# Optimization experiments

Measured on AMD Instinct MI355X. Metric: run time of the kernel, lower is better.

## Reference

```python
import jax, jax.numpy as jnp
import numpy as np
import math

D_MODEL = 1024
N_HEADS = 16
D_K = D_MODEL // N_HEADS


def setup_inputs() -> dict:
    key = jax.random.key(0)
    ks = jax.random.split(key, 9)
    B, N = 2, 8192
    s = 1.0 / math.sqrt(D_MODEL)
    x = jax.random.normal(ks[0], (B, N, D_MODEL), dtype=jnp.float32)
    Wq = jax.random.normal(ks[1], (D_MODEL, D_MODEL), dtype=jnp.float32) * s
    bq = jnp.zeros((D_MODEL,), dtype=jnp.float32)
    Wk = jax.random.normal(ks[2], (D_MODEL, D_MODEL), dtype=jnp.float32) * s
    bk = jnp.zeros((D_MODEL,), dtype=jnp.float32)
    Wv = jax.random.normal(ks[3], (D_MODEL, D_MODEL), dtype=jnp.float32) * s
    bv = jnp.zeros((D_MODEL,), dtype=jnp.float32)
    Wo = jax.random.normal(ks[4], (D_MODEL, D_MODEL), dtype=jnp.float32) * s
    bo = jnp.zeros((D_MODEL,), dtype=jnp.float32)
    return {"x": x, "Wq": Wq, "bq": bq, "Wk": Wk, "bk": bk,
            "Wv": Wv, "bv": bv, "Wo": Wo, "bo": bo}


def _fft_circulant_attention(Q, K, V):
    # Q,K,V: (B,H,N,d_k); FFT along the sequence axis (axis=2)
    B, H, N, d_k = Q.shape
    scale = 1.0 / math.sqrt(d_k)
    Q_fft = jnp.fft.rfft(Q, axis=2)
    K_fft = jnp.fft.rfft(K, axis=2)
    # circular cross-correlation summed over d_k -> (B,H,Nf)
    scores_fft = jnp.sum(Q_fft * jnp.conj(K_fft), axis=-1)
    scores = jnp.fft.irfft(scores_fft, n=N, axis=2) * scale  # (B,H,N)
    attn = jax.nn.softmax(scores, axis=-1)                    # (B,H,N)
    attn_fft = jnp.fft.rfft(attn, axis=2)                     # (B,H,Nf)
    V_fft = jnp.fft.rfft(V, axis=2)                           # (B,H,Nf,d_k)
    out_fft = attn_fft[..., None] * V_fft
    return jnp.fft.irfft(out_fft, n=N, axis=2)                # (B,H,N,d_k)


def reference(x, Wq, bq, Wk, bk, Wv, bv, Wo, bo):
    B, N, _ = x.shape
    # torch Linear: x @ W.T + b
    def proj(W, b):
        return (x @ W.T + b).reshape(B, N, N_HEADS, D_K).transpose(0, 2, 1, 3)
    Q = proj(Wq, bq)
    K = proj(Wk, bk)
    V = proj(Wv, bv)
    O = _fft_circulant_attention(Q, K, V)          # (B,H,N,d_k)
    O = O.transpose(0, 2, 1, 3).reshape(B, N, D_MODEL)
    return O @ Wo.T + bo
```

## Files before the change

kernel.cpp:

```cpp
#include <hip/hip_runtime.h>
#include <math.h>
#include <stdint.h>

#define NDIM 8192
#define LOG2N 13
#define DM 1024
#define NH 16
#define DKH 64
#define BATCH 2
#define NSPLIT 16
#define NPT (NDIM / 256)

typedef __attribute__((ext_vector_type(8))) short short8v;
typedef __attribute__((ext_vector_type(4))) float f32x4;

__device__ inline float bf2f(unsigned short u) {
  return __uint_as_float(((unsigned int)u) << 16);
}
__device__ inline unsigned short f2bf(float f) {
  unsigned int u = __float_as_uint(f);
  u += 0x7fffu + ((u >> 16) & 1u);
  return (unsigned short)(u >> 16);
}
__device__ inline float2 cmul(float2 a, float2 b) {
  return make_float2(a.x * b.x - a.y * b.y, a.x * b.y + a.y * b.x);
}
__device__ inline float2 cmulc(float2 a, float2 b) {
  return make_float2(a.x * b.x + a.y * b.y, a.y * b.x - a.x * b.y);
}

__device__ inline void gload_lds16(const void* g, void* l) {
  __builtin_amdgcn_global_load_lds(
      (const __attribute__((address_space(1))) unsigned int*)(uintptr_t)g,
      (__attribute__((address_space(3))) unsigned int*)(uintptr_t)l, 16, 0, 0);
}

__global__ void twiddle_init(float2* tw) {
  int k = blockIdx.x * blockDim.x + threadIdx.x;
  if (k < NDIM) {
    double a = -2.0 * 3.14159265358979323846 * (double)k / (double)NDIM;
    tw[k] = make_float2((float)cos(a), (float)sin(a));
  }
}

__global__ __launch_bounds__(256)
void split_x(const float* __restrict__ x, unsigned short* __restrict__ xhi,
             unsigned short* __restrict__ xlo) {
  size_t i = ((size_t)blockIdx.x * 256 + threadIdx.x) * 4;
  float4 v = *(const float4*)&x[i];
  ushort4 h, l;
  h.x = f2bf(v.x); l.x = f2bf(v.x - bf2f(h.x));
  h.y = f2bf(v.y); l.y = f2bf(v.y - bf2f(h.y));
  h.z = f2bf(v.z); l.z = f2bf(v.z - bf2f(h.z));
  h.w = f2bf(v.w); l.w = f2bf(v.w - bf2f(h.w));
  *(ushort4*)&xhi[i] = h;
  *(ushort4*)&xlo[i] = l;
}

__global__ __launch_bounds__(256)
void split_w(const float* __restrict__ Wq, const float* __restrict__ Wk,
             const float* __restrict__ Wv, const float* __restrict__ Wo,
             unsigned short* __restrict__ whi, unsigned short* __restrict__ wlo,
             unsigned short* __restrict__ wob) {
  int z = blockIdx.z;
  const float* W = (z == 0) ? Wq : ((z == 1) ? Wk : ((z == 2) ? Wv : Wo));
  size_t i = ((size_t)blockIdx.x * 256 + threadIdx.x) * 4;
  float4 v = *(const float4*)&W[i];
  ushort4 h, l;
  h.x = f2bf(v.x); l.x = f2bf(v.x - bf2f(h.x));
  h.y = f2bf(v.y); l.y = f2bf(v.y - bf2f(h.y));
  h.z = f2bf(v.z); l.z = f2bf(v.z - bf2f(h.z));
  h.w = f2bf(v.w); l.w = f2bf(v.w - bf2f(h.w));
  if (z < 3) {
    *(ushort4*)&whi[(size_t)z * DM * DM + i] = h;
    *(ushort4*)&wlo[(size_t)z * DM * DM + i] = l;
  } else {
    *(ushort4*)&wob[i] = h;
  }
}

__device__ inline void fft_fwd(float2* __restrict__ s, const float2* __restrict__ tw, int tid) {
  for (int lm = 11; lm >= 1; lm -= 2) {
    int m = 1 << lm;
    int sh = 11 - lm;
    __syncthreads();
    for (int t = tid; t < NDIM / 4; t += 256) {
      int p = t & (m - 1);
      int i0 = ((t >> lm) << (lm + 2)) + p;
      float2 x0 = s[i0], x1 = s[i0 + m], x2 = s[i0 + 2 * m], x3 = s[i0 + 3 * m];
      float2 a = make_float2(x0.x + x2.x, x0.y + x2.y);
      float2 b = make_float2(x0.x - x2.x, x0.y - x2.y);
      float2 c = make_float2(x1.x + x3.x, x1.y + x3.y);
      float2 d = make_float2(x1.x - x3.x, x1.y - x3.y);
      float2 y0 = make_float2(a.x + c.x, a.y + c.y);
      float2 y2 = make_float2(a.x - c.x, a.y - c.y);
      float2 y1 = make_float2(b.x + d.y, b.y - d.x);
      float2 y3 = make_float2(b.x - d.y, b.y + d.x);
      int e = p << sh;
      s[i0] = y0;
      s[i0 + m]     = cmul(y1, tw[e]);
      s[i0 + 2 * m] = cmul(y2, tw[2 * e]);
      s[i0 + 3 * m] = cmul(y3, tw[3 * e]);
    }
  }
  __syncthreads();
  for (int t = tid; t < NDIM / 2; t += 256) {
    int i0 = t * 2;
    float2 u = s[i0], v = s[i0 + 1];
    s[i0] = make_float2(u.x + v.x, u.y + v.y);
    s[i0 + 1] = make_float2(u.x - v.x, u.y - v.y);
  }
  __syncthreads();
}
__device__ inline void fft_inv(float2* __restrict__ s, const float2* __restrict__ tw, int tid) {
  __syncthreads();
  for (int t = tid; t < NDIM / 2; t += 256) {
    int i0 = t * 2;
    float2 u = s[i0], v = s[i0 + 1];
    s[i0] = make_float2(u.x + v.x, u.y + v.y);
    s[i0 + 1] = make_float2(u.x - v.x, u.y - v.y);
  }
  for (int lm = 1; lm <= 11; lm += 2) {
    int m = 1 << lm;
    int sh = 11 - lm;
    __syncthreads();
    for (int t = tid; t < NDIM / 4; t += 256) {
      int p = t & (m - 1);
      int i0 = ((t >> lm) << (lm + 2)) + p;
      int e = p << sh;
      float2 z0 = s[i0];
      float2 z1 = cmulc(s[i0 + m], tw[e]);
      float2 z2 = cmulc(s[i0 + 2 * m], tw[2 * e]);
      float2 z3 = cmulc(s[i0 + 3 * m], tw[3 * e]);
      float2 a = make_float2(z0.x + z2.x, z0.y + z2.y);
      float2 b = make_float2(z0.x - z2.x, z0.y - z2.y);
      float2 c = make_float2(z1.x + z3.x, z1.y + z3.y);
      float2 d = make_float2(z1.x - z3.x, z1.y - z3.y);
      s[i0]         = make_float2(a.x + c.x, a.y + c.y);
      s[i0 + m]     = make_float2(b.x - d.y, b.y + d.x);
      s[i0 + 2 * m] = make_float2(a.x - c.x, a.y - c.y);
      s[i0 + 3 * m] = make_float2(b.x + d.y, b.y - d.x);
    }
  }
  __syncthreads();
}

__device__ inline float blk_max(float v, float* red, int tid) {
  #pragma unroll
  for (int o = 32; o > 0; o >>= 1) v = fmaxf(v, __shfl_down(v, o, 64));
  __syncthreads();
  if ((tid & 63) == 0) red[tid >> 6] = v;
  __syncthreads();
  float r = fmaxf(fmaxf(red[0], red[1]), fmaxf(red[2], red[3]));
  __syncthreads();
  return r;
}
__device__ inline float blk_sum(float v, float* red, int tid) {
  #pragma unroll
  for (int o = 32; o > 0; o >>= 1) v += __shfl_down(v, o, 64);
  __syncthreads();
  if ((tid & 63) == 0) red[tid >> 6] = v;
  __syncthreads();
  float r = (red[0] + red[1]) + (red[2] + red[3]);
  __syncthreads();
  return r;
}

__global__ __launch_bounds__(256)
void proj_gemm_mfma(const unsigned short* __restrict__ xhi, const unsigned short* __restrict__ xlo,
                    const unsigned short* __restrict__ whi, const unsigned short* __restrict__ wlo,
                    const float* __restrict__ bq, const float* __restrict__ bk,
                    const float* __restrict__ bv,
                    float* __restrict__ Qt, float* __restrict__ Kt, unsigned short* __restrict__ Vt) {
  int z = blockIdx.z;
  int b = z / 3, wsel = z % 3;
  bool full = (wsel < 2);
  const unsigned short* Wh = whi + (size_t)wsel * DM * DM;
  const unsigned short* Wl = wlo + (size_t)wsel * DM * DM;
  const float* bias = (wsel == 0) ? bq : ((wsel == 1) ? bk : bv);
  int cb = blockIdx.y * 128;
  int nb = blockIdx.x * 128;
  __shared__ unsigned short lAh[128 * 64], lAl[128 * 64];
  __shared__ unsigned short lBh[128 * 64], lBl[128 * 64];
  int tid = threadIdx.x;
  int lane = tid & 63, wid = tid >> 6;
  int wr = wid >> 1, wc = wid & 1;
  int srow = tid >> 3, sg = tid & 7;
  const unsigned short* gAh = Wh + (size_t)cb * DM;
  const unsigned short* gAl = Wl + (size_t)cb * DM;
  const unsigned short* gBh = xhi + ((size_t)b * NDIM + nb) * DM;
  const unsigned short* gBl = xlo + ((size_t)b * NDIM + nb) * DM;

  f32x4 acc[4][4];
  #pragma unroll
  for (int i = 0; i < 4; ++i)
    #pragma unroll
    for (int j = 0; j < 4; ++j) acc[i][j] = (f32x4){0.f, 0.f, 0.f, 0.f};

  int col = lane & 15, kg = lane >> 4;
  for (int k0 = 0; k0 < DM; k0 += 64) {
    #pragma unroll
    for (int i = 0; i < 4; ++i) {
      int r = i * 32 + srow;
      int gc = (sg ^ (r & 7)) * 8;
      size_t go = (size_t)r * DM + k0 + gc;
      int lo_ = r * 64 + sg * 8;
      gload_lds16(gAh + go, &lAh[lo_]);
      gload_lds16(gBh + go, &lBh[lo_]);
      if (full) {
        gload_lds16(gAl + go, &lAl[lo_]);
        gload_lds16(gBl + go, &lBl[lo_]);
      }
    }
    asm volatile("s_waitcnt vmcnt(0)");
    __syncthreads();
    #pragma unroll
    for (int kk = 0; kk < 2; ++kk) {
      short8v ah[4], al[4], bh_[4], bl_[4];
      #pragma unroll
      for (int mi = 0; mi < 4; ++mi) {
        int r = wr * 64 + mi * 16 + col;
        int s = r * 64 + (((kk * 4 + kg) ^ (r & 7)) * 8);
        ah[mi] = *(const short8v*)&lAh[s];
        if (full) al[mi] = *(const short8v*)&lAl[s];
      }
      #pragma unroll
      for (int ni = 0; ni < 4; ++ni) {
        int r = wc * 64 + ni * 16 + col;
        int s = r * 64 + (((kk * 4 + kg) ^ (r & 7)) * 8);
        bh_[ni] = *(const short8v*)&lBh[s];
        if (full) bl_[ni] = *(const short8v*)&lBl[s];
      }
      #pragma unroll
      for (int mi = 0; mi < 4; ++mi)
        #pragma unroll
        for (int ni = 0; ni < 4; ++ni) {
          acc[mi][ni] = __builtin_amdgcn_mfma_f32_16x16x32_bf16(ah[mi], bh_[ni], acc[mi][ni], 0, 0, 0);
          if (full) {
            acc[mi][ni] = __builtin_amdgcn_mfma_f32_16x16x32_bf16(ah[mi], bl_[ni], acc[mi][ni], 0, 0, 0);
            acc[mi][ni] = __builtin_amdgcn_mfma_f32_16x16x32_bf16(al[mi], bh_[ni], acc[mi][ni], 0, 0, 0);
          }
        }
    }
    __syncthreads();
  }
  size_t obase = (size_t)b * DM * NDIM;
  #pragma unroll
  for (int mi = 0; mi < 4; ++mi) {
    #pragma unroll
    for (int reg = 0; reg < 4; ++reg) {
      int c = cb + wr * 64 + mi * 16 + kg * 4 + reg;
      float bsv = bias[c];
      #pragma unroll
      for (int ni = 0; ni < 4; ++ni) {
        int n = nb + wc * 64 + ni * 16 + col;
        float v = acc[mi][ni][reg] + bsv;
        if (wsel < 2) {
          float* out = ((wsel == 0) ? Qt : Kt) + obase;
          out[(size_t)c * NDIM + n] = v;
        } else {
          Vt[obase + (size_t)c * NDIM + n] = f2bf(v);
        }
      }
    }
  }
}

__global__ __launch_bounds__(256)
void score_fft_kernel(const float* __restrict__ Qt, const float* __restrict__ Kt,
                      const float2* __restrict__ tw, float2* __restrict__ part) {
  extern __shared__ float2 buf[];
  int bh = blockIdx.x / NSPLIT;
  int split = blockIdx.x % NSPLIT;
  int b = bh / NH, h = bh % NH;
  int tid = threadIdx.x;
  float qfx[NPT], qfy[NPT], accx[NPT], accy[NPT];
  #pragma unroll
  for (int i = 0; i < NPT; ++i) { accx[i] = 0.f; accy[i] = 0.f; }

  for (int dp = 0; dp < 2; ++dp) {
    int c0 = h * DKH + (split * 2 + dp) * 2;
    const float* q0 = Qt + ((size_t)b * DM + c0) * NDIM;
    const float* q1 = q0 + NDIM;
    const float* k0c = Kt + ((size_t)b * DM + c0) * NDIM;
    const float* k1c = k0c + NDIM;
    #pragma unroll
    for (int i = 0; i < NPT; ++i) {
      int ii = i * 256 + tid;
      buf[ii] = make_float2(q0[ii], q1[ii]);
    }
    fft_fwd(buf, tw, tid);
    #pragma unroll
    for (int i = 0; i < NPT; ++i) { float2 v = buf[i * 256 + tid]; qfx[i] = v.x; qfy[i] = v.y; }
    #pragma unroll
    for (int i = 0; i < NPT; ++i) {
      int ii = i * 256 + tid;
      buf[ii] = make_float2(k0c[ii], k1c[ii]);
    }
    fft_fwd(buf, tw, tid);
    #pragma unroll
    for (int i = 0; i < NPT; ++i) {
      float2 kf = buf[i * 256 + tid];
      accx[i] += qfx[i] * kf.x + qfy[i] * kf.y;
      accy[i] += qfy[i] * kf.x - qfx[i] * kf.y;
    }
  }
  float2* dst = part + ((size_t)bh * NSPLIT + split) * NDIM;
  #pragma unroll
  for (int i = 0; i < NPT; ++i) dst[i * 256 + tid] = make_float2(accx[i], accy[i]);
}

__global__ __launch_bounds__(256)
void softmax_attn_kernel(const float2* __restrict__ part, const float2* __restrict__ tw,
                         float2* __restrict__ attnf) {
  extern __shared__ float2 buf[];
  int bh = blockIdx.x;
  int tid = threadIdx.x;
  for (int i = tid; i < NDIM; i += 256) {
    float sx = 0.f, sy = 0.f;
    #pragma unroll
    for (int s = 0; s < NSPLIT; ++s) {
      float2 v = part[((size_t)bh * NSPLIT + s) * NDIM + i];
      sx += v.x; sy += v.y;
    }
    buf[i] = make_float2(sx, sy);
  }
  fft_inv(buf, tw, tid);
  const float scale = 0.125f / (float)NDIM;
  float vals[NPT];
  float lmax = -3.0e38f;
  #pragma unroll
  for (int i = 0; i < NPT; ++i) {
    float v = buf[i * 256 + tid].x * scale;
    vals[i] = v;
    lmax = fmaxf(lmax, v);
  }
  float* red = (float*)buf;
  float gmax = blk_max(lmax, red, tid);
  float lsum = 0.f;
  #pragma unroll
  for (int i = 0; i < NPT; ++i) { float e = expf(vals[i] - gmax); vals[i] = e; lsum += e; }
  float gsum = blk_sum(lsum, red, tid);
  float inv = 1.0f / gsum;
  #pragma unroll
  for (int i = 0; i < NPT; ++i) buf[i * 256 + tid] = make_float2(vals[i] * inv, 0.f);
  fft_fwd(buf, tw, tid);
  for (int i = tid; i < NDIM; i += 256) attnf[(size_t)bh * NDIM + i] = buf[i];
}

__global__ __launch_bounds__(256)
void out_fft_kernel(const unsigned short* __restrict__ Vt, const float2* __restrict__ attnf,
                    const float2* __restrict__ tw, unsigned short* __restrict__ Ot) {
  extern __shared__ float2 buf[];
  int idx = blockIdx.x;
  int b = idx / (DM / 2), cp = idx % (DM / 2);
  int c0 = cp * 2;
  int h = c0 >> 6;
  int bh = b * NH + h;
  int tid = threadIdx.x;
  const unsigned short* v0 = Vt + ((size_t)b * DM + c0) * NDIM;
  const unsigned short* v1 = v0 + NDIM;
  for (int i = tid; i < NDIM; i += 256) buf[i] = make_float2(bf2f(v0[i]), bf2f(v1[i]));
  fft_fwd(buf, tw, tid);
  for (int i = tid; i < NDIM; i += 256) {
    float2 vf = buf[i];
    float2 af = attnf[(size_t)bh * NDIM + i];
    buf[i] = cmul(vf, af);
  }
  fft_inv(buf, tw, tid);
  const float invn = 1.0f / (float)NDIM;
  unsigned short* o0 = Ot + ((size_t)b * DM + c0) * NDIM;
  unsigned short* o1 = o0 + NDIM;
  for (int i = tid; i < NDIM; i += 256) {
    float2 v = buf[i];
    o0[i] = f2bf(v.x * invn);
    o1[i] = f2bf(v.y * invn);
  }
}

__global__ __launch_bounds__(256)
void transpose_ot(const unsigned short* __restrict__ Ot, unsigned short* __restrict__ Ont) {
  int b = blockIdx.z;
  int cb = blockIdx.y * 64, n0 = blockIdx.x * 64;
  __shared__ unsigned short t[64][68];
  int tid = threadIdx.x;
  int r = tid >> 4, c4 = (tid & 15) * 4;
  const unsigned short* src = Ot + (size_t)b * DM * NDIM;
  #pragma unroll
  for (int i = 0; i < 4; ++i) {
    ushort4 v = *(const ushort4*)&src[(size_t)(cb + i * 16 + r) * NDIM + n0 + c4];
    *(ushort4*)&t[i * 16 + r][c4] = v;
  }
  __syncthreads();
  unsigned short* dst = Ont + (size_t)b * NDIM * DM;
  #pragma unroll
  for (int i = 0; i < 4; ++i) {
    int n = i * 16 + r;
    ushort4 v;
    v.x = t[c4 + 0][n]; v.y = t[c4 + 1][n]; v.z = t[c4 + 2][n]; v.w = t[c4 + 3][n];
    *(ushort4*)&dst[(size_t)(n0 + n) * DM + cb + c4] = v;
  }
}

__global__ __launch_bounds__(256)
void final_gemm_mfma(const unsigned short* __restrict__ Ont, const unsigned short* __restrict__ Wob,
                     const float* __restrict__ bo, float* __restrict__ out) {
  int b = blockIdx.z;
  int nb = blockIdx.x * 128;
  int pb = blockIdx.y * 128;
  __shared__ unsigned short lA[128 * 64], lB[128 * 64];
  int tid = threadIdx.x;
  int lane = tid & 63, wid = tid >> 6;
  int wr = wid >> 1, wc = wid & 1;
  int srow = tid >> 3, sg = tid & 7;
  const unsigned short* gA = Ont + ((size_t)b * NDIM + nb) * DM;
  const unsigned short* gB = Wob + (size_t)pb * DM;

  f32x4 acc[4][4];
  #pragma unroll
  for (int i = 0; i < 4; ++i)
    #pragma unroll
    for (int j = 0; j < 4; ++j) acc[i][j] = (f32x4){0.f, 0.f, 0.f, 0.f};

  int col = lane & 15, kg = lane >> 4;
  for (int k0 = 0; k0 < DM; k0 += 64) {
    #pragma unroll
    for (int i = 0; i < 4; ++i) {
      int r = i * 32 + srow;
      int gc = (sg ^ (r & 7)) * 8;
      size_t go = (size_t)r * DM + k0 + gc;
      int lo_ = r * 64 + sg * 8;
      gload_lds16(gA + go, &lA[lo_]);
      gload_lds16(gB + go, &lB[lo_]);
    }
    asm volatile("s_waitcnt vmcnt(0)");
    __syncthreads();
    #pragma unroll
    for (int kk = 0; kk < 2; ++kk) {
      short8v af[4], bf[4];
      #pragma unroll
      for (int mi = 0; mi < 4; ++mi) {
        int r = wr * 64 + mi * 16 + col;
        af[mi] = *(const short8v*)&lA[r * 64 + (((kk * 4 + kg) ^ (r & 7)) * 8)];
      }
      #pragma unroll
      for (int ni = 0; ni < 4; ++ni) {
        int r = wc * 64 + ni * 16 + col;
        bf[ni] = *(const short8v*)&lB[r * 64 + (((kk * 4 + kg) ^ (r & 7)) * 8)];
      }
      #pragma unroll
      for (int mi = 0; mi < 4; ++mi)
        #pragma unroll
        for (int ni = 0; ni < 4; ++ni)
          acc[mi][ni] = __builtin_amdgcn_mfma_f32_16x16x32_bf16(af[mi], bf[ni], acc[mi][ni], 0, 0, 0);
    }
    __syncthreads();
  }
  #pragma unroll
  for (int mi = 0; mi < 4; ++mi) {
    #pragma unroll
    for (int reg = 0; reg < 4; ++reg) {
      int n = nb + wr * 64 + mi * 16 + kg * 4 + reg;
      size_t rowoff = ((size_t)b * NDIM + n) * DM;
      #pragma unroll
      for (int ni = 0; ni < 4; ++ni) {
        int cp = pb + wc * 64 + ni * 16 + col;
        out[rowoff + cp] = acc[mi][ni][reg] + bo[cp];
      }
    }
  }
}

extern "C" void kernel_launch(void* const* d_in, const int* in_sizes, int n_in,
                              void* d_out, int out_size, void* d_ws, size_t ws_size,
                              hipStream_t stream) {
  (void)in_sizes; (void)n_in; (void)out_size;
  const float* x  = (const float*)d_in[0];
  const float* Wq = (const float*)d_in[1]; const float* bq = (const float*)d_in[2];
  const float* Wk = (const float*)d_in[3]; const float* bk = (const float*)d_in[4];
  const float* Wv = (const float*)d_in[5]; const float* bv = (const float*)d_in[6];
  const float* Wo = (const float*)d_in[7]; const float* bo = (const float*)d_in[8];

  char* ws = (char*)d_ws;
  size_t off = 0;
  float2* tw = (float2*)(ws + off); off += (size_t)NDIM * sizeof(float2);
  float*  Qt = (float*)(ws + off);  off += (size_t)BATCH * DM * NDIM * 4;
  float*  Kt = (float*)(ws + off);  off += (size_t)BATCH * DM * NDIM * 4;
  unsigned short* Vt  = (unsigned short*)(ws + off); off += (size_t)BATCH * DM * NDIM * 2;
  size_t xhi_off = off;
  unsigned short* Xhi = (unsigned short*)(ws + off); off += (size_t)BATCH * NDIM * DM * 2;
  size_t xlo_off = off;
  unsigned short* Xlo = (unsigned short*)(ws + off); off += (size_t)BATCH * NDIM * DM * 2;
  unsigned short* Whi = (unsigned short*)(ws + off); off += (size_t)3 * DM * DM * 2;
  unsigned short* Wlo = (unsigned short*)(ws + off); off += (size_t)3 * DM * DM * 2;
  unsigned short* Wob = (unsigned short*)(ws + off); off += (size_t)DM * DM * 2;
  float2* part  = (float2*)(ws + xhi_off);
  float2* attnf = (float2*)(ws + xlo_off);
  unsigned short* Ot  = (unsigned short*)Qt;
  unsigned short* Ont = (unsigned short*)Kt;

  if (ws_size < off) return;

  twiddle_init<<<32, 256, 0, stream>>>(tw);
  split_x<<<(BATCH * NDIM * DM) / (256 * 4), 256, 0, stream>>>(x, Xhi, Xlo);
  split_w<<<dim3((DM * DM) / (256 * 4), 1, 4), 256, 0, stream>>>(Wq, Wk, Wv, Wo, Whi, Wlo, Wob);

  dim3 pg(NDIM / 128, DM / 128, 3 * BATCH);
  proj_gemm_mfma<<<pg, 256, 0, stream>>>(Xhi, Xlo, Whi, Wlo, bq, bk, bv, Qt, Kt, Vt);

  score_fft_kernel<<<BATCH * NH * NSPLIT, 256, NDIM * sizeof(float2), stream>>>(Qt, Kt, tw, part);
  softmax_attn_kernel<<<BATCH * NH, 256, NDIM * sizeof(float2), stream>>>(part, tw, attnf);
  out_fft_kernel<<<BATCH * DM / 2, 256, NDIM * sizeof(float2), stream>>>(Vt, attnf, tw, Ot);

  transpose_ot<<<dim3(NDIM / 64, DM / 64, BATCH), 256, 0, stream>>>(Ot, Ont);
  final_gemm_mfma<<<dim3(NDIM / 128, DM / 128, BATCH), 256, 0, stream>>>(Ont, Wob, bo, (float*)d_out);
}
```

Baseline: 528.9 us.

## Use radix-8 FFT stages and split partial-sum reduction into its own kernel

Replaces the radix-4 shared-memory FFT passes with radix-8 butterflies, so the 8192-point transform takes four radix-8 passes plus a radix-2 pass instead of six radix-4 passes plus a radix-2 pass. This means fewer barriers and fewer LDS round trips per FFT, at the cost of more registers per thread. Separately, the sum over split partial score spectra moves out of the 32-block softmax kernel into a wide grid-parallel reduction kernel. That spreads the memory-bound reduction across many more CUs, but adds an extra kernel launch and an intermediate buffer.

```diff
diff --git a/kernel.cpp b/kernel.cpp
--- a/kernel.cpp
+++ b/kernel.cpp
@@ -3,7 +3,6 @@
 #include <stdint.h>
 
 #define NDIM 8192
-#define LOG2N 13
 #define DM 1024
 #define NH 16
 #define DKH 64
@@ -80,66 +79,100 @@
 }
 
 __device__ inline void fft_fwd(float2* __restrict__ s, const float2* __restrict__ tw, int tid) {
-  for (int lm = 11; lm >= 1; lm -= 2) {
+  const float C = 0.70710678118654752f;
+  for (int lm = 10; lm >= 1; lm -= 3) {
     int m = 1 << lm;
-    int sh = 11 - lm;
+    int sh = 10 - lm;
     __syncthreads();
-    for (int t = tid; t < NDIM / 4; t += 256) {
+    for (int t = tid; t < NDIM / 8; t += 256) {
       int p = t & (m - 1);
-      int i0 = ((t >> lm) << (lm + 2)) + p;
-      float2 x0 = s[i0], x1 = s[i0 + m], x2 = s[i0 + 2 * m], x3 = s[i0 + 3 * m];
-      float2 a = make_float2(x0.x + x2.x, x0.y + x2.y);
-      float2 b = make_float2(x0.x - x2.x, x0.y - x2.y);
-      float2 c = make_float2(x1.x + x3.x, x1.y + x3.y);
-      float2 d = make_float2(x1.x - x3.x, x1.y - x3.y);
-      float2 y0 = make_float2(a.x + c.x, a.y + c.y);
-      float2 y2 = make_float2(a.x - c.x, a.y - c.y);
-      float2 y1 = make_float2(b.x + d.y, b.y - d.x);
-      float2 y3 = make_float2(b.x - d.y, b.y + d.x);
+      int i0 = ((t >> lm) << (lm + 3)) + p;
+      float2 x0 = s[i0],       x1 = s[i0 + m],     x2 = s[i0 + 2 * m], x3 = s[i0 + 3 * m];
+      float2 x4 = s[i0 + 4 * m], x5 = s[i0 + 5 * m], x6 = s[i0 + 6 * m], x7 = s[i0 + 7 * m];
+      float2 e0 = {x0.x + x4.x, x0.y + x4.y}, o0 = {x0.x - x4.x, x0.y - x4.y};
+      float2 e1 = {x1.x + x5.x, x1.y + x5.y}, o1 = {x1.x - x5.x, x1.y - x5.y};
+      float2 e2 = {x2.x + x6.x, x2.y + x6.y}, o2 = {x2.x - x6.x, x2.y - x6.y};
+      float2 e3 = {x3.x + x7.x, x3.y + x7.y}, o3 = {x3.x - x7.x, x3.y - x7.y};
+      float2 t1 = {C * (o1.x + o1.y), C * (o1.y - o1.x)};
+      float2 t2 = {o2.y, -o2.x};
+      float2 t3 = {C * (o3.y - o3.x), -C * (o3.x + o3.y)};
+      float2 pe = {e0.x + e2.x, e0.y + e2.y}, qe = {e0.x - e2.x, e0.y - e2.y};
+      float2 re = {e1.x + e3.x, e1.y + e3.y}, se = {e1.x - e3.x, e1.y - e3.y};
+      float2 po = {o0.x + t2.x, o0.y + t2.y}, qo = {o0.x - t2.x, o0.y - t2.y};
+      float2 ro = {t1.x + t3.x, t1.y + t3.y}, so = {t1.x - t3.x, t1.y - t3.y};
+      float2 y0 = {pe.x + re.x, pe.y + re.y};
+      float2 y4 = {pe.x - re.x, pe.y - re.y};
+      float2 y2 = {qe.x + se.y, qe.y - se.x};
+      float2 y6 = {qe.x - se.y, qe.y + se.x};
+      float2 y1 = {po.x + ro.x, po.y + ro.y};
+      float2 y5 = {po.x - ro.x, po.y - ro.y};
+      float2 y3 = {qo.x + so.y, qo.y - so.x};
+      float2 y7 = {qo.x - so.y, qo.y + so.x};
       int e = p << sh;
-      s[i0] = y0;
+      s[i0]         = y0;
       s[i0 + m]     = cmul(y1, tw[e]);
       s[i0 + 2 * m] = cmul(y2, tw[2 * e]);
       s[i0 + 3 * m] = cmul(y3, tw[3 * e]);
+      s[i0 + 4 * m] = cmul(y4, tw[4 * e]);
+      s[i0 + 5 * m] = cmul(y5, tw[5 * e]);
+      s[i0 + 6 * m] = cmul(y6, tw[6 * e]);
+      s[i0 + 7 * m] = cmul(y7, tw[7 * e]);
     }
   }
   __syncthreads();
   for (int t = tid; t < NDIM / 2; t += 256) {
     int i0 = t * 2;
     float2 u = s[i0], v = s[i0 + 1];
-    s[i0] = make_float2(u.x + v.x, u.y + v.y);
+    s[i0]     = make_float2(u.x + v.x, u.y + v.y);
     s[i0 + 1] = make_float2(u.x - v.x, u.y - v.y);
   }
   __syncthreads();
 }
+
 __device__ inline void fft_inv(float2* __restrict__ s, const float2* __restrict__ tw, int tid) {
+  const float C = 0.70710678118654752f;
   __syncthreads();
   for (int t = tid; t < NDIM / 2; t += 256) {
     int i0 = t * 2;
     float2 u = s[i0], v = s[i0 + 1];
-    s[i0] = make_float2(u.x + v.x, u.y + v.y);
+    s[i0]     = make_float2(u.x + v.x, u.y + v.y);
     s[i0 + 1] = make_float2(u.x - v.x, u.y - v.y);
   }
-  for (int lm = 1; lm <= 11; lm += 2) {
+  for (int lm = 1; lm <= 10; lm += 3) {
     int m = 1 << lm;
-    int sh = 11 - lm;
+    int sh = 10 - lm;
     __syncthreads();
-    for (int t = tid; t < NDIM / 4; t += 256) {
+    for (int t = tid; t < NDIM / 8; t += 256) {
       int p = t & (m - 1);
-      int i0 = ((t >> lm) << (lm + 2)) + p;
+      int i0 = ((t >> lm) << (lm + 3)) + p;
       int e = p << sh;
       float2 z0 = s[i0];
-      float2 z1 = cmulc(s[i0 + m], tw[e]);
+      float2 z1 = cmulc(s[i0 + m],     tw[e]);
       float2 z2 = cmulc(s[i0 + 2 * m], tw[2 * e]);
       float2 z3 = cmulc(s[i0 + 3 * m], tw[3 * e]);
-      float2 a = make_float2(z0.x + z2.x, z0.y + z2.y);
-      float2 b = make_float2(z0.x - z2.x, z0.y - z2.y);
-      float2 c = make_float2(z1.x + z3.x, z1.y + z3.y);
-      float2 d = make_float2(z1.x - z3.x, z1.y - z3.y);
-      s[i0]         = make_float2(a.x + c.x, a.y + c.y);
-      s[i0 + m]     = make_float2(b.x - d.y, b.y + d.x);
-      s[i0 + 2 * m] = make_float2(a.x - c.x, a.y - c.y);
-      s[i0 + 3 * m] = make_float2(b.x + d.y, b.y - d.x);
+      float2 z4 = cmulc(s[i0 + 4 * m], tw[4 * e]);
+      float2 z5 = cmulc(s[i0 + 5 * m], tw[5 * e]);
+      float2 z6 = cmulc(s[i0 + 6 * m], tw[6 * e]);
+      float2 z7 = cmulc(s[i0 + 7 * m], tw[7 * e]);
+      float2 E0 = {z0.x + z4.x, z0.y + z4.y}, O0 = {z0.x - z4.x, z0.y - z4.y};
+      float2 E1 = {z1.x + z5.x, z1.y + z5.y}, O1 = {z1.x - z5.x, z1.y - z5.y};
+      float2 E2 = {z2.x + z6.x, z2.y + z6.y}, O2 = {z2.x - z6.x, z2.y - z6.y};
+      float2 E3 = {z3.x + z7.x, z3.y + z7.y}, O3 = {z3.x - z7.x, z3.y - z7.y};
+      float2 T1 = {C * (O1.x - O1.y), C * (O1.x + O1.y)};
+      float2 T2 = {-O2.y, O2.x};
+      float2 T3 = {-C * (O3.x + O3.y), C * (O3.x - O3.y)};
+      float2 PE = {E0.x + E2.x, E0.y + E2.y}, QE = {E0.x - E2.x, E0.y - E2.y};
+      float2 RE = {E1.x + E3.x, E1.y + E3.y}, SE = {E1.x - E3.x, E1.y - E3.y};
+      float2 PO = {O0.x + T2.x, O0.y + T2.y}, QO = {O0.x - T2.x, O0.y - T2.y};
+      float2 RO = {T1.x + T3.x, T1.y + T3.y}, SO = {T1.x - T3.x, T1.y - T3.y};
+      s[i0]         = make_float2(PE.x + RE.x, PE.y + RE.y);
+      s[i0 + 4 * m] = make_float2(PE.x - RE.x, PE.y - RE.y);
+      s[i0 + 2 * m] = make_float2(QE.x - SE.y, QE.y + SE.x);
+      s[i0 + 6 * m] = make_float2(QE.x + SE.y, QE.y - SE.x);
+      s[i0 + m]     = make_float2(PO.x + RO.x, PO.y + RO.y);
+      s[i0 + 5 * m] = make_float2(PO.x - RO.x, PO.y - RO.y);
+      s[i0 + 3 * m] = make_float2(QO.x - SO.y, QO.y + SO.x);
+      s[i0 + 7 * m] = make_float2(QO.x + SO.y, QO.y - SO.x);
     }
   }
   __syncthreads();
@@ -311,20 +344,29 @@
 }
 
 __global__ __launch_bounds__(256)
-void softmax_attn_kernel(const float2* __restrict__ part, const float2* __restrict__ tw,
+void reduce_part(const float2* __restrict__ part, float2* __restrict__ sred) {
+  #pragma unroll
+  for (int rep = 0; rep < 2; ++rep) {
+    size_t g = (size_t)blockIdx.x * 512 + rep * 256 + threadIdx.x;
+    int bh = (int)(g >> 13);
+    int i  = (int)(g & (NDIM - 1));
+    float sx = 0.f, sy = 0.f;
+    #pragma unroll
+    for (int s = 0; s < NSPLIT; ++s) {
+      float2 v = part[((size_t)bh * NSPLIT + s) * NDIM + i];
+      sx += v.x; sy += v.y;
+    }
+    sred[g] = make_float2(sx, sy);
+  }
+}
+
+__global__ __launch_bounds__(256)
+void softmax_attn_kernel(const float2* __restrict__ sred, const float2* __restrict__ tw,
                          float2* __restrict__ attnf) {
   extern __shared__ float2 buf[];
   int bh = blockIdx.x;
   int tid = threadIdx.x;
-  for (int i = tid; i < NDIM; i += 256) {
-    float sx = 0.f, sy = 0.f;
-    #pragma unroll
-    for (int s = 0; s < NSPLIT; ++s) {
-      float2 v = part[((size_t)bh * NSPLIT + s) * NDIM + i];
-      sx += v.x; sy += v.y;
-    }
-    buf[i] = make_float2(sx, sy);
-  }
+  for (int i = tid; i < NDIM; i += 256) buf[i] = sred[(size_t)bh * NDIM + i];
   fft_inv(buf, tw, tid);
   const float scale = 0.125f / (float)NDIM;
   float vals[NPT];
@@ -496,6 +538,7 @@
   unsigned short* Wob = (unsigned short*)(ws + off); off += (size_t)DM * DM * 2;
   float2* part  = (float2*)(ws + xhi_off);
   float2* attnf = (float2*)(ws + xlo_off);
+  float2* sred  = (float2*)(ws + xlo_off + 4194304);
   unsigned short* Ot  = (unsigned short*)Qt;
   unsigned short* Ont = (unsigned short*)Kt;
 
@@ -509,7 +552,8 @@
   proj_gemm_mfma<<<pg, 256, 0, stream>>>(Xhi, Xlo, Whi, Wlo, bq, bk, bv, Qt, Kt, Vt);
 
   score_fft_kernel<<<BATCH * NH * NSPLIT, 256, NDIM * sizeof(float2), stream>>>(Qt, Kt, tw, part);
-  softmax_attn_kernel<<<BATCH * NH, 256, NDIM * sizeof(float2), stream>>>(part, tw, attnf);
+  reduce_part<<<(BATCH * NH * NDIM) / 512, 256, 0, stream>>>(part, sred);
+  softmax_attn_kernel<<<BATCH * NH, 256, NDIM * sizeof(float2), stream>>>(sred, tw, attnf);
   out_fft_kernel<<<BATCH * DM / 2, 256, NDIM * sizeof(float2), stream>>>(Vt, attnf, tw, Ot);
 
   transpose_ot<<<dim3(NDIM / 64, DM / 64, BATCH), 256, 0, stream>>>(Ot, Ont);
```

New measurement: 517.9 us. 1.02x faster.
